# Kernel optimization log

Hardware: AMD Instinct MI355X
Metric: run time of the kernel (lower is better)

Reference implementation:

```python
import jax, jax.numpy as jnp
import numpy as np
from jax import lax

H = 300  # L1 = L2 = 300 in the source


def setup_inputs() -> dict:
    key = jax.random.key(0)
    ks = jax.random.split(key, 10)
    B = 1024
    oplen = 256
    s = 1.0 / np.sqrt(H)
    return {
        "h0": jax.random.normal(ks[0], (B, H), jnp.float32),
        "c0": jax.random.normal(ks[1], (B, H), jnp.float32),
        "start": jax.random.normal(ks[2], (B, H), jnp.float32),
        # LSTMCell params (PyTorch layout: [4H, H] weights, [4H] biases; gate order i,f,g,o)
        "W_ih": jax.random.normal(ks[3], (4 * H, H), jnp.float32) * s,
        "W_hh": jax.random.normal(ks[4], (4 * H, H), jnp.float32) * s,
        "b_ih": jax.random.normal(ks[5], (4 * H,), jnp.float32) * s,
        "b_hh": jax.random.normal(ks[6], (4 * H,), jnp.float32) * s,
        # output Linear [H, H]
        "W_out": jax.random.normal(ks[7], (H, H), jnp.float32) * s,
        "b_out": jax.random.normal(ks[8], (H,), jnp.float32) * s,
        "oplen": oplen,
    }


def reference(h0, c0, start, W_ih, W_hh, b_ih, b_hh, W_out, b_out, oplen):
    def step(carry, _):
        h, c, x = carry
        # LSTMCell: gates = x W_ih^T + b_ih + h W_hh^T + b_hh
        gates = x @ W_ih.T + b_ih + h @ W_hh.T + b_hh  # [B, 4H]
        i, f, g, o = jnp.split(gates, 4, axis=-1)
        i = jax.nn.sigmoid(i)
        f = jax.nn.sigmoid(f)
        g = jnp.tanh(g)
        o = jax.nn.sigmoid(o)
        c_new = f * c + i * g
        h_new = o * jnp.tanh(c_new)
        out = h_new @ W_out.T + b_out  # fed back as next input
        return (h_new, c_new, out), out

    _, outs = lax.scan(step, (h0, c0, start), None, length=oplen)
    return outs  # [oplen, B, H]
```

## Files before the change

### kernel.cpp

```cpp
#include <hip/hip_runtime.h>
#include <hip/hip_bf16.h>


typedef __attribute__((ext_vector_type(8))) short bf16x8;
typedef __attribute__((ext_vector_type(4))) float f32x4;

__device__ __forceinline__ float sigf(float x) { return 1.0f / (1.0f + __expf(-x)); }
__device__ __forceinline__ float tanh_fast(float x) { return 2.0f / (1.0f + __expf(-2.0f * x)) - 1.0f; }
__device__ __forceinline__ short f2bf(float x) { __hip_bfloat16 h = __float2bfloat16(x); return *(short*)&h; }
__device__ __forceinline__ float bf2f(short s) { __hip_bfloat16 h; *(short*)&h = s; return __bfloat162float(h); }

__global__ void build_kernel(const float* __restrict__ W_out, const float* __restrict__ b_out,
                             float* __restrict__ W_big, float* __restrict__ bias_big,
                             unsigned int* __restrict__ hfrag_zero) {
    int stride = gridDim.x * blockDim.x;
    int idx = blockIdx.x * blockDim.x + threadIdx.x;
    for (int i = idx; i < 655360; i += stride) hfrag_zero[i] = 0u;
    for (int i = idx; i < 300 * 300; i += stride) W_big[1200 * 300 + i] = W_out[i];
    for (int i = idx; i < 300; i += stride) bias_big[1200 + i] = b_out[i];
}

__global__ __launch_bounds__(128) void fold_kernel(const float* __restrict__ W_ih,
                                                   const float* __restrict__ W_hh,
                                                   const float* __restrict__ W_out,
                                                   float* __restrict__ W_big) {
    int j = blockIdx.x;
    __shared__ float row[300];
    for (int m = threadIdx.x; m < 300; m += 128) row[m] = W_ih[j * 300 + m];
    __syncthreads();
    int k0 = threadIdx.x, k1 = threadIdx.x + 128, k2 = threadIdx.x + 256;
    float a0 = 0.f, a1 = 0.f, a2 = 0.f;
    for (int m = 0; m < 300; ++m) {
        float w = row[m];
        a0 += w * W_out[m * 300 + k0];
        a1 += w * W_out[m * 300 + k1];
        if (k2 < 300) a2 += w * W_out[m * 300 + k2];
    }
    W_big[j * 300 + k0] = W_hh[j * 300 + k0] + a0;
    W_big[j * 300 + k1] = W_hh[j * 300 + k1] + a1;
    if (k2 < 300) W_big[j * 300 + k2] = W_hh[j * 300 + k2] + a2;
}

__global__ __launch_bounds__(64) void bias_fold_kernel(const float* __restrict__ W_ih,
                                                       const float* __restrict__ b_ih,
                                                       const float* __restrict__ b_hh,
                                                       const float* __restrict__ b_out,
                                                       float* __restrict__ bias_big) {
    int j = blockIdx.x;
    int lane = threadIdx.x;
    float s = 0.f;
    for (int m = lane; m < 300; m += 64) s += W_ih[j * 300 + m] * b_out[m];
    for (int off = 32; off > 0; off >>= 1) s += __shfl_down(s, off);
    if (lane == 0) bias_big[j] = b_ih[j] + b_hh[j] + s;
}

__global__ __launch_bounds__(64) void pack_w_kernel(const float* __restrict__ W_big,
                                                    short* __restrict__ Wh, short* __restrict__ Wl) {
    int tile = blockIdx.x;
    int jt = tile / 50;
    int rem = tile - jt * 50;
    int ch = rem / 10;
    int kc = rem - ch * 10;
    int lane = threadIdx.x;
    int j = jt * 16 + (lane & 15);
    int kbase = kc * 32 + (lane >> 4) * 8;
    int r = (ch < 4) ? (ch * 300 + j) : (1200 + j);
    size_t base = (size_t)tile * 512 + (size_t)lane * 8;
#pragma unroll
    for (int jj = 0; jj < 8; ++jj) {
        int k = kbase + jj;
        float v = (j < 300 && k < 300) ? W_big[(size_t)r * 300 + k] : 0.f;
        short hi = f2bf(v);
        short lo = f2bf(v - bf2f(hi));
        Wh[base + jj] = hi;
        Wl[base + jj] = lo;
    }
}

__global__ __launch_bounds__(128) void step0_kernel(
    const float* __restrict__ x_in, const float* __restrict__ h_in,
    const float* __restrict__ W_ih, const float* __restrict__ W_hh,
    const float* __restrict__ b_ih, const float* __restrict__ b_hh,
    const float* __restrict__ c_in, float* __restrict__ c_out,
    float* __restrict__ h_out) {
    __shared__ float hs[16][68];
    __shared__ float wsm[16][32];
    const int t = threadIdx.x;
    const int bm0 = blockIdx.x * 64;
    const int jg0 = blockIdx.y * 8;

    const int row_idx = t & 31;
    const int wkq = (t >> 5) << 2;
    const int jl = row_idx >> 2, g = row_idx & 3;
    const int grow = jg0 + jl + 300 * g;
    const bool wvalid = (jg0 + jl) < 300;

    float acc[4][4];
#pragma unroll
    for (int i = 0; i < 4; ++i)
#pragma unroll
        for (int q = 0; q < 4; ++q) acc[i][q] = 0.f;

    for (int it = 0; it < 38; ++it) {
        const int k0 = it << 4;
#pragma unroll
        for (int q = 0; q < 2; ++q) {
            int qi = t + q * 128;
            int bl = qi >> 2;
            int kq = (qi & 3) << 2;
            int kg = k0 + kq;
            float4 hv = make_float4(0.f, 0.f, 0.f, 0.f);
            if (kg < 600) {
                const float* src = (kg < 300) ? (x_in + (size_t)(bm0 + bl) * 300 + kg)
                                              : (h_in + (size_t)(bm0 + bl) * 300 + (kg - 300));
                hv = *(const float4*)src;
            }
            hs[kq + 0][bl] = hv.x;
            hs[kq + 1][bl] = hv.y;
            hs[kq + 2][bl] = hv.z;
            hs[kq + 3][bl] = hv.w;
        }
        {
            int kg = k0 + wkq;
            float4 wv = make_float4(0.f, 0.f, 0.f, 0.f);
            if (wvalid && kg < 600) {
                const float* src = (kg < 300) ? (W_ih + (size_t)grow * 300 + kg)
                                              : (W_hh + (size_t)grow * 300 + (kg - 300));
                wv = *(const float4*)src;
            }
            wsm[wkq + 0][row_idx] = wv.x;
            wsm[wkq + 1][row_idx] = wv.y;
            wsm[wkq + 2][row_idx] = wv.z;
            wsm[wkq + 3][row_idx] = wv.w;
        }
        __syncthreads();
        const int bs4 = (t & 15) << 2;
        const int c4 = (t >> 4) << 2;
#pragma unroll
        for (int k = 0; k < 16; ++k) {
            float4 hv = *(const float4*)&hs[k][bs4];
            float4 wv = *(const float4*)&wsm[k][c4];
            float hvv[4] = {hv.x, hv.y, hv.z, hv.w};
            float wvv[4] = {wv.x, wv.y, wv.z, wv.w};
#pragma unroll
            for (int bi = 0; bi < 4; ++bi)
#pragma unroll
                for (int q = 0; q < 4; ++q) acc[bi][q] += hvv[bi] * wvv[q];
        }
        __syncthreads();
    }

    const int b0 = bm0 + ((t & 15) << 2);
    const int j = jg0 + (t >> 4);
    if (j < 300) {
        const float bi_ = b_ih[j] + b_hh[j];
        const float bf_ = b_ih[j + 300] + b_hh[j + 300];
        const float bg_ = b_ih[j + 600] + b_hh[j + 600];
        const float bo_ = b_ih[j + 900] + b_hh[j + 900];
#pragma unroll
        for (int bi = 0; bi < 4; ++bi) {
            const int b = b0 + bi;
            float ig = sigf(acc[bi][0] + bi_);
            float fg = sigf(acc[bi][1] + bf_);
            float gg = tanh_fast(acc[bi][2] + bg_);
            float og = sigf(acc[bi][3] + bo_);
            float cn = fg * c_in[(size_t)b * 300 + j] + ig * gg;
            c_out[(size_t)b * 300 + j] = cn;
            h_out[(size_t)b * 300 + j] = og * tanh_fast(cn);
        }
    }
}

__global__ __launch_bounds__(256) void convert_h_kernel(const float* __restrict__ h_row,
                                                        short* __restrict__ Hh, short* __restrict__ Hl) {
    int idx = blockIdx.x * 256 + threadIdx.x;
    int m = idx / 320;
    int k = idx - m * 320;
    float v = (k < 300) ? h_row[(size_t)m * 300 + k] : 0.f;
    short hi = f2bf(v);
    short lo = f2bf(v - bf2f(hi));
    int chunk = k >> 5;
    int lane = (m & 15) + 16 * ((k & 31) >> 3);
    int slot = k & 7;
    size_t fi = (((size_t)(m >> 4) * 10 + chunk) * 64 + lane) * 8 + slot;
    Hh[fi] = hi;
    Hl[fi] = lo;
}

__global__ __launch_bounds__(192, 2) void step_kernel(
    const short* __restrict__ Ah, const short* __restrict__ Al,
    short* __restrict__ Bh, short* __restrict__ Bl,
    const short* __restrict__ Wh, const short* __restrict__ Wl,
    const float* __restrict__ bias,
    float* __restrict__ c_st,
    float* __restrict__ y_out) {
    const int bid = blockIdx.x;
    const int jt = bid >> 5;
    const int mxp = bid & 31;
    const int tid = threadIdx.x;
    const int wave = tid >> 6;
    const int lane = tid & 63;

    __shared__ short As_h[2 * 10 * 512];
    __shared__ short As_l[2 * 10 * 512];
    __shared__ float gbuf[4][32][16];

    {
        const size_t abase = (size_t)(mxp * 2) * 10 * 512;
        const int4* gAh = (const int4*)(Ah + abase);
        const int4* gAl = (const int4*)(Al + abase);
        int4* sAh = (int4*)As_h;
        int4* sAl = (int4*)As_l;
        for (int i = tid; i < 1280; i += 192) {
            sAh[i] = gAh[i];
            sAl[i] = gAl[i];
        }
    }
    __syncthreads();

    const short* aoff_h = As_h + lane * 8;
    const short* aoff_l = As_l + lane * 8;

    if (wave < 2) {
        const int ch0 = wave * 2;
        f32x4 acc[2][2];
#pragma unroll
        for (int a = 0; a < 2; ++a)
#pragma unroll
            for (int b = 0; b < 2; ++b) acc[a][b] = (f32x4){0.f, 0.f, 0.f, 0.f};

        const short* wb_h[2] = {Wh + ((size_t)(jt * 5 + ch0) * 10) * 512 + lane * 8,
                                Wh + ((size_t)(jt * 5 + ch0 + 1) * 10) * 512 + lane * 8};
        const short* wb_l[2] = {Wl + ((size_t)(jt * 5 + ch0) * 10) * 512 + lane * 8,
                                Wl + ((size_t)(jt * 5 + ch0 + 1) * 10) * 512 + lane * 8};
#pragma unroll 2
        for (int kc = 0; kc < 10; ++kc) {
            bf16x8 a0h = *(const bf16x8*)(aoff_h + kc * 512);
            bf16x8 a0l = *(const bf16x8*)(aoff_l + kc * 512);
            bf16x8 a1h = *(const bf16x8*)(aoff_h + (10 + kc) * 512);
            bf16x8 a1l = *(const bf16x8*)(aoff_l + (10 + kc) * 512);
#pragma unroll
            for (int chl = 0; chl < 2; ++chl) {
                bf16x8 bh = *(const bf16x8*)(wb_h[chl] + kc * 512);
                bf16x8 bl = *(const bf16x8*)(wb_l[chl] + kc * 512);
                acc[chl][0] = __builtin_amdgcn_mfma_f32_16x16x32_bf16(a0h, bh, acc[chl][0], 0, 0, 0);
                acc[chl][0] = __builtin_amdgcn_mfma_f32_16x16x32_bf16(a0l, bh, acc[chl][0], 0, 0, 0);
                acc[chl][0] = __builtin_amdgcn_mfma_f32_16x16x32_bf16(a0h, bl, acc[chl][0], 0, 0, 0);
                acc[chl][1] = __builtin_amdgcn_mfma_f32_16x16x32_bf16(a1h, bh, acc[chl][1], 0, 0, 0);
                acc[chl][1] = __builtin_amdgcn_mfma_f32_16x16x32_bf16(a1l, bh, acc[chl][1], 0, 0, 0);
                acc[chl][1] = __builtin_amdgcn_mfma_f32_16x16x32_bf16(a1h, bl, acc[chl][1], 0, 0, 0);
            }
        }
        const int jl = lane & 15;
        const int mr = (lane >> 4) * 4;
#pragma unroll
        for (int chl = 0; chl < 2; ++chl)
#pragma unroll
            for (int mt = 0; mt < 2; ++mt)
#pragma unroll
                for (int r = 0; r < 4; ++r)
                    gbuf[ch0 + chl][mt * 16 + mr + r][jl] = acc[chl][mt][r];
    } else {
        f32x4 accy[2];
        accy[0] = (f32x4){0.f, 0.f, 0.f, 0.f};
        accy[1] = (f32x4){0.f, 0.f, 0.f, 0.f};
        const short* wy = Wh + ((size_t)(jt * 5 + 4) * 10) * 512 + lane * 8;
#pragma unroll 2
        for (int kc = 0; kc < 10; ++kc) {
            bf16x8 a0h = *(const bf16x8*)(aoff_h + kc * 512);
            bf16x8 a0l = *(const bf16x8*)(aoff_l + kc * 512);
            bf16x8 a1h = *(const bf16x8*)(aoff_h + (10 + kc) * 512);
            bf16x8 a1l = *(const bf16x8*)(aoff_l + (10 + kc) * 512);
            bf16x8 bh = *(const bf16x8*)(wy + kc * 512);
            accy[0] = __builtin_amdgcn_mfma_f32_16x16x32_bf16(a0h, bh, accy[0], 0, 0, 0);
            accy[0] = __builtin_amdgcn_mfma_f32_16x16x32_bf16(a0l, bh, accy[0], 0, 0, 0);
            accy[1] = __builtin_amdgcn_mfma_f32_16x16x32_bf16(a1h, bh, accy[1], 0, 0, 0);
            accy[1] = __builtin_amdgcn_mfma_f32_16x16x32_bf16(a1l, bh, accy[1], 0, 0, 0);
        }
        const int j = jt * 16 + (lane & 15);
        if (j < 300) {
            const float by = bias[1200 + j];
            const int mr = (lane >> 4) * 4;
#pragma unroll
            for (int mt = 0; mt < 2; ++mt)
#pragma unroll
                for (int r = 0; r < 4; ++r) {
                    const int m = mxp * 32 + mt * 16 + mr + r;
                    y_out[(size_t)m * 300 + j] = accy[mt][r] + by;
                }
        }
    }
    __syncthreads();

    for (int e = tid; e < 512; e += 192) {
        const int ml = e >> 4;
        const int jl = e & 15;
        const int j = jt * 16 + jl;
        if (j >= 300) continue;
        const int m = mxp * 32 + ml;
        float gi = gbuf[0][ml][jl] + bias[j];
        float gf = gbuf[1][ml][jl] + bias[300 + j];
        float gg = gbuf[2][ml][jl] + bias[600 + j];
        float go = gbuf[3][ml][jl] + bias[900 + j];
        float iv = sigf(gi), fv = sigf(gf), gv = tanh_fast(gg), ov = sigf(go);
        const size_t cj = (size_t)m * 300 + j;
        float cn = fv * c_st[cj] + iv * gv;
        c_st[cj] = cn;
        float hv = ov * tanh_fast(cn);
        short hb = f2bf(hv);
        short lb = f2bf(hv - bf2f(hb));
        const int chunk = j >> 5;
        const int lane_a = (m & 15) + 16 * ((j & 31) >> 3);
        const int slot = j & 7;
        const size_t fi = (((size_t)(m >> 4) * 10 + chunk) * 64 + lane_a) * 8 + slot;
        Bh[fi] = hb;
        Bl[fi] = lb;
    }
}

extern "C" void kernel_launch(void* const* d_in, const int* in_sizes, int n_in,
                              void* d_out, int out_size, void* d_ws, size_t ws_size,
                              hipStream_t stream) {
    const float* h0 = (const float*)d_in[0];
    const float* c0 = (const float*)d_in[1];
    const float* start = (const float*)d_in[2];
    const float* W_ih = (const float*)d_in[3];
    const float* W_hh = (const float*)d_in[4];
    const float* b_ih = (const float*)d_in[5];
    const float* b_hh = (const float*)d_in[6];
    const float* W_out = (const float*)d_in[7];
    const float* b_out = (const float*)d_in[8];
    float* out = (float*)d_out;

    float* wsf = (float*)d_ws;
    float* W_big = wsf;
    float* bias_big = wsf + 450000;
    float* c_ws = wsf + 451504;
    float* h_row = wsf + 758704;
    short* wss = (short*)(wsf + 1065904);
    short* Wh = wss;
    short* Wl = wss + 486400;
    short* H0h = wss + 972800;
    short* H0l = wss + 1300480;
    short* H1h = wss + 1628160;
    short* H1l = wss + 1955840;

    build_kernel<<<2816, 256, 0, stream>>>(W_out, b_out, W_big, bias_big, (unsigned int*)H0h);
    fold_kernel<<<1200, 128, 0, stream>>>(W_ih, W_hh, W_out, W_big);
    bias_fold_kernel<<<1200, 64, 0, stream>>>(W_ih, b_ih, b_hh, b_out, bias_big);
    pack_w_kernel<<<950, 64, 0, stream>>>(W_big, Wh, Wl);

    step0_kernel<<<dim3(16, 38), 128, 0, stream>>>(start, h0, W_ih, W_hh, b_ih, b_hh,
                                                   c0, c_ws, h_row);
    convert_h_kernel<<<1280, 256, 0, stream>>>(h_row, H0h, H0l);

    short* Hb[2][2] = {{H0h, H0l}, {H1h, H1l}};
    for (int tt = 1; tt <= 256; ++tt) {
        short** A = Hb[(tt - 1) & 1];
        short** Bn = Hb[tt & 1];
        step_kernel<<<608, 192, 0, stream>>>(A[0], A[1], Bn[0], Bn[1], Wh, Wl,
                                             bias_big, c_ws,
                                             out + (size_t)(tt - 1) * 307200);
    }
}
```

Before: 2.424 ms.

## Replace per-step launches with persistent kernel using grid barrier and LDS-resident weights

Replaces the 256 per-timestep step_kernel launches with one persistent kernel of 247 blocks that loops over all timesteps, separated by a global atomic barrier. Each block keeps its weight slice (hi/lo bf16) in LDS, keeps its cell state in registers, and double-buffers loading of the h fragments from global memory into LDS. The tiling changes to 80 rows by 16 columns per block. This removes launch overhead and repeated weight/c-state traffic, at the cost of a spin barrier whose correctness depends on all 247 blocks being co-resident.

```diff
diff --git a/kernel.cpp b/kernel.cpp
--- a/kernel.cpp
+++ b/kernel.cpp
@@ -4,6 +4,8 @@
 
 typedef __attribute__((ext_vector_type(8))) short bf16x8;
 typedef __attribute__((ext_vector_type(4))) float f32x4;
+
+#define MFMA16(a, b, c) __builtin_amdgcn_mfma_f32_16x16x32_bf16((a), (b), (c), 0, 0, 0)
 
 __device__ __forceinline__ float sigf(float x) { return 1.0f / (1.0f + __expf(-x)); }
 __device__ __forceinline__ float tanh_fast(float x) { return 2.0f / (1.0f + __expf(-2.0f * x)) - 1.0f; }
@@ -12,12 +14,13 @@
 
 __global__ void build_kernel(const float* __restrict__ W_out, const float* __restrict__ b_out,
                              float* __restrict__ W_big, float* __restrict__ bias_big,
-                             unsigned int* __restrict__ hfrag_zero) {
+                             unsigned int* __restrict__ hfrag_zero, unsigned int* __restrict__ bar) {
     int stride = gridDim.x * blockDim.x;
     int idx = blockIdx.x * blockDim.x + threadIdx.x;
-    for (int i = idx; i < 655360; i += stride) hfrag_zero[i] = 0u;
+    for (int i = idx; i < 665600; i += stride) hfrag_zero[i] = 0u;
     for (int i = idx; i < 300 * 300; i += stride) W_big[1200 * 300 + i] = W_out[i];
     for (int i = idx; i < 300; i += stride) bias_big[1200 + i] = b_out[i];
+    if (idx < 64) bar[idx] = 0u;
 }
 
 __global__ __launch_bounds__(128) void fold_kernel(const float* __restrict__ W_ih,
@@ -187,134 +190,227 @@
     Hl[fi] = lo;
 }
 
-__global__ __launch_bounds__(192, 2) void step_kernel(
-    const short* __restrict__ Ah, const short* __restrict__ Al,
-    short* __restrict__ Bh, short* __restrict__ Bl,
-    const short* __restrict__ Wh, const short* __restrict__ Wl,
-    const float* __restrict__ bias,
-    float* __restrict__ c_st,
-    float* __restrict__ y_out) {
+__global__ __launch_bounds__(256, 1) void persist_kernel(
+    short* __restrict__ H0h, short* __restrict__ H0l,
+    short* __restrict__ H1h, short* __restrict__ H1l,
+    const short* __restrict__ Wph, const short* __restrict__ Wpl,
+    const float* __restrict__ bias, const float* __restrict__ c_init,
+    float* __restrict__ out, unsigned int* __restrict__ bar) {
+    __shared__ __align__(16) short w_hi[5 * 10 * 512];
+    __shared__ __align__(16) short w_lo[4 * 10 * 512];
+    __shared__ __align__(16) short a_sm[2 * 2 * 2 * 5 * 512];
+    __shared__ float gbuf[5][80][17];
+    __shared__ float bias_s[80];
+
     const int bid = blockIdx.x;
-    const int jt = bid >> 5;
-    const int mxp = bid & 31;
+    const int seq = (bid & 7) * 31 + (bid >> 3);
+    const int mg = seq / 19;
+    const int jt = seq - mg * 19;
     const int tid = threadIdx.x;
     const int wave = tid >> 6;
     const int lane = tid & 63;
 
-    __shared__ short As_h[2 * 10 * 512];
-    __shared__ short As_l[2 * 10 * 512];
-    __shared__ float gbuf[4][32][16];
-
     {
-        const size_t abase = (size_t)(mxp * 2) * 10 * 512;
-        const int4* gAh = (const int4*)(Ah + abase);
-        const int4* gAl = (const int4*)(Al + abase);
-        int4* sAh = (int4*)As_h;
-        int4* sAl = (int4*)As_l;
-        for (int i = tid; i < 1280; i += 192) {
-            sAh[i] = gAh[i];
-            sAl[i] = gAl[i];
-        }
-    }
-    __syncthreads();
-
-    const short* aoff_h = As_h + lane * 8;
-    const short* aoff_l = As_l + lane * 8;
-
-    if (wave < 2) {
-        const int ch0 = wave * 2;
-        f32x4 acc[2][2];
-#pragma unroll
-        for (int a = 0; a < 2; ++a)
-#pragma unroll
-            for (int b = 0; b < 2; ++b) acc[a][b] = (f32x4){0.f, 0.f, 0.f, 0.f};
-
-        const short* wb_h[2] = {Wh + ((size_t)(jt * 5 + ch0) * 10) * 512 + lane * 8,
-                                Wh + ((size_t)(jt * 5 + ch0 + 1) * 10) * 512 + lane * 8};
-        const short* wb_l[2] = {Wl + ((size_t)(jt * 5 + ch0) * 10) * 512 + lane * 8,
-                                Wl + ((size_t)(jt * 5 + ch0 + 1) * 10) * 512 + lane * 8};
-#pragma unroll 2
-        for (int kc = 0; kc < 10; ++kc) {
-            bf16x8 a0h = *(const bf16x8*)(aoff_h + kc * 512);
-            bf16x8 a0l = *(const bf16x8*)(aoff_l + kc * 512);
-            bf16x8 a1h = *(const bf16x8*)(aoff_h + (10 + kc) * 512);
-            bf16x8 a1l = *(const bf16x8*)(aoff_l + (10 + kc) * 512);
-#pragma unroll
-            for (int chl = 0; chl < 2; ++chl) {
-                bf16x8 bh = *(const bf16x8*)(wb_h[chl] + kc * 512);
-                bf16x8 bl = *(const bf16x8*)(wb_l[chl] + kc * 512);
-                acc[chl][0] = __builtin_amdgcn_mfma_f32_16x16x32_bf16(a0h, bh, acc[chl][0], 0, 0, 0);
-                acc[chl][0] = __builtin_amdgcn_mfma_f32_16x16x32_bf16(a0l, bh, acc[chl][0], 0, 0, 0);
-                acc[chl][0] = __builtin_amdgcn_mfma_f32_16x16x32_bf16(a0h, bl, acc[chl][0], 0, 0, 0);
-                acc[chl][1] = __builtin_amdgcn_mfma_f32_16x16x32_bf16(a1h, bh, acc[chl][1], 0, 0, 0);
-                acc[chl][1] = __builtin_amdgcn_mfma_f32_16x16x32_bf16(a1l, bh, acc[chl][1], 0, 0, 0);
-                acc[chl][1] = __builtin_amdgcn_mfma_f32_16x16x32_bf16(a1h, bl, acc[chl][1], 0, 0, 0);
-            }
-        }
-        const int jl = lane & 15;
-        const int mr = (lane >> 4) * 4;
-#pragma unroll
-        for (int chl = 0; chl < 2; ++chl)
-#pragma unroll
-            for (int mt = 0; mt < 2; ++mt)
-#pragma unroll
-                for (int r = 0; r < 4; ++r)
-                    gbuf[ch0 + chl][mt * 16 + mr + r][jl] = acc[chl][mt][r];
-    } else {
-        f32x4 accy[2];
-        accy[0] = (f32x4){0.f, 0.f, 0.f, 0.f};
-        accy[1] = (f32x4){0.f, 0.f, 0.f, 0.f};
-        const short* wy = Wh + ((size_t)(jt * 5 + 4) * 10) * 512 + lane * 8;
-#pragma unroll 2
-        for (int kc = 0; kc < 10; ++kc) {
-            bf16x8 a0h = *(const bf16x8*)(aoff_h + kc * 512);
-            bf16x8 a0l = *(const bf16x8*)(aoff_l + kc * 512);
-            bf16x8 a1h = *(const bf16x8*)(aoff_h + (10 + kc) * 512);
-            bf16x8 a1l = *(const bf16x8*)(aoff_l + (10 + kc) * 512);
-            bf16x8 bh = *(const bf16x8*)(wy + kc * 512);
-            accy[0] = __builtin_amdgcn_mfma_f32_16x16x32_bf16(a0h, bh, accy[0], 0, 0, 0);
-            accy[0] = __builtin_amdgcn_mfma_f32_16x16x32_bf16(a0l, bh, accy[0], 0, 0, 0);
-            accy[1] = __builtin_amdgcn_mfma_f32_16x16x32_bf16(a1h, bh, accy[1], 0, 0, 0);
-            accy[1] = __builtin_amdgcn_mfma_f32_16x16x32_bf16(a1l, bh, accy[1], 0, 0, 0);
-        }
-        const int j = jt * 16 + (lane & 15);
-        if (j < 300) {
-            const float by = bias[1200 + j];
-            const int mr = (lane >> 4) * 4;
-#pragma unroll
-            for (int mt = 0; mt < 2; ++mt)
-#pragma unroll
-                for (int r = 0; r < 4; ++r) {
-                    const int m = mxp * 32 + mt * 16 + mr + r;
-                    y_out[(size_t)m * 300 + j] = accy[mt][r] + by;
-                }
-        }
-    }
-    __syncthreads();
-
-    for (int e = tid; e < 512; e += 192) {
-        const int ml = e >> 4;
-        const int jl = e & 15;
+        const int4* s1 = (const int4*)(Wph + (size_t)jt * 25600);
+        int4* d1 = (int4*)w_hi;
+        for (int i = tid; i < 3200; i += 256) d1[i] = s1[i];
+        const int4* s2 = (const int4*)(Wpl + (size_t)jt * 25600);
+        int4* d2 = (int4*)w_lo;
+        for (int i = tid; i < 2560; i += 256) d2[i] = s2[i];
+        if (tid < 80) {
+            const int cch = tid >> 4, jl = tid & 15;
+            const int j = jt * 16 + jl;
+            bias_s[tid] = (j < 300) ? bias[cch * 300 + j] : 0.f;
+        }
+    }
+
+    float c_reg[5];
+#pragma unroll
+    for (int k = 0; k < 5; ++k) {
+        const int e = tid + (k << 8);
+        const int ml = e >> 4, jl = e & 15;
         const int j = jt * 16 + jl;
-        if (j >= 300) continue;
-        const int m = mxp * 32 + ml;
-        float gi = gbuf[0][ml][jl] + bias[j];
-        float gf = gbuf[1][ml][jl] + bias[300 + j];
-        float gg = gbuf[2][ml][jl] + bias[600 + j];
-        float go = gbuf[3][ml][jl] + bias[900 + j];
-        float iv = sigf(gi), fv = sigf(gf), gv = tanh_fast(gg), ov = sigf(go);
-        const size_t cj = (size_t)m * 300 + j;
-        float cn = fv * c_st[cj] + iv * gv;
-        c_st[cj] = cn;
-        float hv = ov * tanh_fast(cn);
-        short hb = f2bf(hv);
-        short lb = f2bf(hv - bf2f(hb));
-        const int chunk = j >> 5;
-        const int lane_a = (m & 15) + 16 * ((j & 31) >> 3);
-        const int slot = j & 7;
-        const size_t fi = (((size_t)(m >> 4) * 10 + chunk) * 64 + lane_a) * 8 + slot;
-        Bh[fi] = hb;
-        Bl[fi] = lb;
+        const int m = mg * 80 + ml;
+        c_reg[k] = (j < 300 && m < 1024) ? c_init[(size_t)m * 300 + j] : 0.f;
+    }
+
+    const int chb = (wave >> 1) << 1;
+    const int gmlo = (wave & 1) ? 3 : 0;
+    const int gcnt = (wave & 1) ? 2 : 3;
+    const int ycnt = (wave == 1) ? 2 : ((wave == 3) ? 3 : 0);
+    const int ymlo = (wave == 1) ? 3 : 0;
+
+    const short* whB = w_hi + chb * 5120 + (lane << 3);
+    const short* wlB = w_lo + chb * 5120 + (lane << 3);
+    const short* wyB = w_hi + 4 * 5120 + (lane << 3);
+    const short* aB = a_sm + (lane << 3);
+
+    const int jlc = lane & 15;
+    const int mr = ((lane >> 4) << 2);
+
+#pragma unroll 1
+    for (int tt = 1; tt <= 256; ++tt) {
+        const short* Ah = (tt & 1) ? H0h : H1h;
+        const short* Al = (tt & 1) ? H0l : H1l;
+        short* Bh = (tt & 1) ? H1h : H0h;
+        short* Bl = (tt & 1) ? H1l : H0l;
+        float* yo = out + (size_t)(tt - 1) * 307200;
+
+        f32x4 acc[2][3];
+        f32x4 accy[3];
+#pragma unroll
+        for (int c = 0; c < 2; ++c)
+#pragma unroll
+            for (int i = 0; i < 3; ++i) acc[c][i] = (f32x4){0.f, 0.f, 0.f, 0.f};
+#pragma unroll
+        for (int i = 0; i < 3; ++i) accy[i] = (f32x4){0.f, 0.f, 0.f, 0.f};
+
+        {
+            int4 st[5];
+#pragma unroll
+            for (int i = 0; i < 5; ++i) {
+                const int o = wave + (i << 2);
+                const int mt = o % 5, prec = (o / 5) & 1, kcL = o / 10;
+                const short* src = prec ? Al : Ah;
+                st[i] = ((const int4*)(src + ((size_t)((mg * 5 + mt) * 10 + kcL) << 9)))[lane];
+            }
+#pragma unroll
+            for (int i = 0; i < 5; ++i) {
+                const int o = wave + (i << 2);
+                const int mt = o % 5, prec = (o / 5) & 1, kcL = o / 10;
+                ((int4*)(a_sm + ((size_t)((((kcL << 1) | prec) * 5 + mt)) << 9)))[lane] = st[i];
+            }
+        }
+        __syncthreads();
+
+#pragma unroll
+        for (int nc = 0; nc < 5; ++nc) {
+            const int rb = nc & 1;
+            int4 st[5];
+            if (nc < 4) {
+#pragma unroll
+                for (int i = 0; i < 5; ++i) {
+                    const int o = wave + (i << 2);
+                    const int mt = o % 5, prec = (o / 5) & 1, kcL = o / 10;
+                    const short* src = prec ? Al : Ah;
+                    st[i] = ((const int4*)(src +
+                              ((size_t)((mg * 5 + mt) * 10 + (nc * 2 + 2 + kcL)) << 9)))[lane];
+                }
+            }
+#pragma unroll
+            for (int kcL = 0; kcL < 2; ++kcL) {
+                const int kc = nc * 2 + kcL;
+                const bf16x8 bh0 = *(const bf16x8*)(whB + (kc << 9));
+                const bf16x8 bh1 = *(const bf16x8*)(whB + ((10 + kc) << 9));
+                const bf16x8 bl0 = *(const bf16x8*)(wlB + (kc << 9));
+                const bf16x8 bl1 = *(const bf16x8*)(wlB + ((10 + kc) << 9));
+                const short* ab = aB + (((rb << 1) | kcL) * 5120);
+#pragma unroll
+                for (int mti = 0; mti < 3; ++mti) {
+                    if (mti < gcnt) {
+                        const int mt = gmlo + mti;
+                        const bf16x8 ah = *(const bf16x8*)(ab + (mt << 9));
+                        const bf16x8 al = *(const bf16x8*)(ab + ((5 + mt) << 9));
+                        acc[0][mti] = MFMA16(ah, bh0, acc[0][mti]);
+                        acc[0][mti] = MFMA16(al, bh0, acc[0][mti]);
+                        acc[0][mti] = MFMA16(ah, bl0, acc[0][mti]);
+                        acc[1][mti] = MFMA16(ah, bh1, acc[1][mti]);
+                        acc[1][mti] = MFMA16(al, bh1, acc[1][mti]);
+                        acc[1][mti] = MFMA16(ah, bl1, acc[1][mti]);
+                    }
+                }
+                if (ycnt) {
+                    const bf16x8 byh = *(const bf16x8*)(wyB + (kc << 9));
+#pragma unroll
+                    for (int yi = 0; yi < 3; ++yi) {
+                        if (yi < ycnt) {
+                            const int mt = ymlo + yi;
+                            const bf16x8 ah = *(const bf16x8*)(ab + (mt << 9));
+                            const bf16x8 al = *(const bf16x8*)(ab + ((5 + mt) << 9));
+                            accy[yi] = MFMA16(ah, byh, accy[yi]);
+                            accy[yi] = MFMA16(al, byh, accy[yi]);
+                        }
+                    }
+                }
+            }
+            if (nc < 4) {
+                const int wb = rb ^ 1;
+#pragma unroll
+                for (int i = 0; i < 5; ++i) {
+                    const int o = wave + (i << 2);
+                    const int mt = o % 5, prec = (o / 5) & 1, kcL = o / 10;
+                    ((int4*)(a_sm + ((size_t)(((((wb << 1) | kcL) << 1) | prec) * 5 + mt) << 9)))[lane] = st[i];
+                }
+            }
+            __syncthreads();
+        }
+
+#pragma unroll
+        for (int c = 0; c < 2; ++c)
+#pragma unroll
+            for (int mti = 0; mti < 3; ++mti) {
+                if (mti < gcnt) {
+#pragma unroll
+                    for (int r = 0; r < 4; ++r)
+                        gbuf[chb + c][(gmlo + mti) * 16 + mr + r][jlc] = acc[c][mti][r];
+                }
+            }
+        if (ycnt) {
+#pragma unroll
+            for (int yi = 0; yi < 3; ++yi) {
+                if (yi < ycnt) {
+#pragma unroll
+                    for (int r = 0; r < 4; ++r)
+                        gbuf[4][(ymlo + yi) * 16 + mr + r][jlc] = accy[yi][r];
+                }
+            }
+        }
+        __syncthreads();
+
+#pragma unroll
+        for (int k = 0; k < 5; ++k) {
+            const int e = tid + (k << 8);
+            const int ml = e >> 4, jl = e & 15;
+            const int j = jt * 16 + jl;
+            const int m = mg * 80 + ml;
+            if (j < 300 && m < 1024) {
+                const float gi = gbuf[0][ml][jl] + bias_s[jl];
+                const float gf = gbuf[1][ml][jl] + bias_s[16 + jl];
+                const float gg = gbuf[2][ml][jl] + bias_s[32 + jl];
+                const float go_ = gbuf[3][ml][jl] + bias_s[48 + jl];
+                const float iv = sigf(gi), fv = sigf(gf), gv = tanh_fast(gg), ov = sigf(go_);
+                const float cn = fv * c_reg[k] + iv * gv;
+                c_reg[k] = cn;
+                const float hv = ov * tanh_fast(cn);
+                const float yv = gbuf[4][ml][jl] + bias_s[64 + jl];
+                __builtin_nontemporal_store(yv, yo + (size_t)m * 300 + j);
+                const short hb = f2bf(hv);
+                const short lb = f2bf(hv - bf2f(hb));
+                const int chk = j >> 5;
+                const int lane_a = (m & 15) + (((j & 31) >> 3) << 4);
+                const int slot = j & 7;
+                const size_t fi = ((((size_t)(m >> 4) * 10 + chk) << 6) + lane_a) * 8 + slot;
+                __builtin_nontemporal_store(hb, Bh + fi);
+                __builtin_nontemporal_store(lb, Bl + fi);
+            }
+        }
+
+        __syncthreads();
+        if (tid == 0) {
+            __threadfence();
+            const unsigned prev =
+                __hip_atomic_fetch_add(&bar[0], 1u, __ATOMIC_RELAXED, __HIP_MEMORY_SCOPE_AGENT);
+            if (prev == (unsigned)(247 * tt - 1)) {
+                __hip_atomic_store(&bar[32], (unsigned)tt, __ATOMIC_RELAXED, __HIP_MEMORY_SCOPE_AGENT);
+            } else {
+                while (__hip_atomic_load(&bar[32], __ATOMIC_RELAXED, __HIP_MEMORY_SCOPE_AGENT) <
+                       (unsigned)tt) {
+                    __builtin_amdgcn_s_sleep(2);
+                }
+            }
+            __threadfence();
+        }
+        __syncthreads();
     }
 }
 
@@ -341,11 +437,12 @@
     short* Wh = wss;
     short* Wl = wss + 486400;
     short* H0h = wss + 972800;
-    short* H0l = wss + 1300480;
-    short* H1h = wss + 1628160;
-    short* H1l = wss + 1955840;
-
-    build_kernel<<<2816, 256, 0, stream>>>(W_out, b_out, W_big, bias_big, (unsigned int*)H0h);
+    short* H0l = wss + 1305600;
+    short* H1h = wss + 1638400;
+    short* H1l = wss + 1971200;
+    unsigned int* bar = (unsigned int*)(wss + 2304000);
+
+    build_kernel<<<2816, 256, 0, stream>>>(W_out, b_out, W_big, bias_big, (unsigned int*)H0h, bar);
     fold_kernel<<<1200, 128, 0, stream>>>(W_ih, W_hh, W_out, W_big);
     bias_fold_kernel<<<1200, 64, 0, stream>>>(W_ih, b_ih, b_hh, b_out, bias_big);
     pack_w_kernel<<<950, 64, 0, stream>>>(W_big, Wh, Wl);
@@ -354,12 +451,6 @@
                                                    c0, c_ws, h_row);
     convert_h_kernel<<<1280, 256, 0, stream>>>(h_row, H0h, H0l);
 
-    short* Hb[2][2] = {{H0h, H0l}, {H1h, H1l}};
-    for (int tt = 1; tt <= 256; ++tt) {
-        short** A = Hb[(tt - 1) & 1];
-        short** Bn = Hb[tt & 1];
-        step_kernel<<<608, 192, 0, stream>>>(A[0], A[1], Bn[0], Bn[1], Wh, Wl,
-                                             bias_big, c_ws,
-                                             out + (size_t)(tt - 1) * 307200);
-    }
-}
+    persist_kernel<<<247, 256, 0, stream>>>(H0h, H0l, H1h, H1l, Wh, Wl,
+                                            bias_big, c_ws, out, bar);
+}
```

Measured after the change: 5.927 ms. +144.5%, slower.

## Replace per-step launches with persistent kernel using per-group flag synchronization

Applied to the files above, without the earlier changes.

Swaps 256 separate step launches for one persistent kernel of 152 blocks. Blocks are split into 8 groups of 19, each owning 128 batch rows, and the blocks of a group coordinate through atomic step flags in global memory. Each block keeps its slice of the packed weights in LDS and the cell state in registers. The aim is to remove per-step launch overhead and the repeated weight and state reloads, at the cost of spin-wait polling and reliance on all blocks being co-resident.

```diff
diff --git a/kernel.cpp b/kernel.cpp
--- a/kernel.cpp
+++ b/kernel.cpp
@@ -4,6 +4,8 @@
 
 typedef __attribute__((ext_vector_type(8))) short bf16x8;
 typedef __attribute__((ext_vector_type(4))) float f32x4;
+
+#define MFMA16(a, b, c) __builtin_amdgcn_mfma_f32_16x16x32_bf16((a), (b), (c), 0, 0, 0)
 
 __device__ __forceinline__ float sigf(float x) { return 1.0f / (1.0f + __expf(-x)); }
 __device__ __forceinline__ float tanh_fast(float x) { return 2.0f / (1.0f + __expf(-2.0f * x)) - 1.0f; }
@@ -12,12 +14,13 @@
 
 __global__ void build_kernel(const float* __restrict__ W_out, const float* __restrict__ b_out,
                              float* __restrict__ W_big, float* __restrict__ bias_big,
-                             unsigned int* __restrict__ hfrag_zero) {
+                             unsigned int* __restrict__ hfrag_zero, unsigned int* __restrict__ flags) {
     int stride = gridDim.x * blockDim.x;
     int idx = blockIdx.x * blockDim.x + threadIdx.x;
     for (int i = idx; i < 655360; i += stride) hfrag_zero[i] = 0u;
     for (int i = idx; i < 300 * 300; i += stride) W_big[1200 * 300 + i] = W_out[i];
     for (int i = idx; i < 300; i += stride) bias_big[1200 + i] = b_out[i];
+    if (idx < 256) flags[idx] = 0u;
 }
 
 __global__ __launch_bounds__(128) void fold_kernel(const float* __restrict__ W_ih,
@@ -187,134 +190,174 @@
     Hl[fi] = lo;
 }
 
-__global__ __launch_bounds__(192, 2) void step_kernel(
-    const short* __restrict__ Ah, const short* __restrict__ Al,
-    short* __restrict__ Bh, short* __restrict__ Bl,
-    const short* __restrict__ Wh, const short* __restrict__ Wl,
-    const float* __restrict__ bias,
-    float* __restrict__ c_st,
-    float* __restrict__ y_out) {
+__global__ __launch_bounds__(256, 1) void persist_kernel(
+    short* __restrict__ H0h, short* __restrict__ H0l,
+    short* __restrict__ H1h, short* __restrict__ H1l,
+    const short* __restrict__ Wph, const short* __restrict__ Wpl,
+    const float* __restrict__ bias, const float* __restrict__ c_init,
+    float* __restrict__ out, unsigned* __restrict__ flags) {
+    __shared__ __align__(16) short w_hi[50 * 512];
+    __shared__ __align__(16) short w_lo[40 * 512];
+
     const int bid = blockIdx.x;
-    const int jt = bid >> 5;
-    const int mxp = bid & 31;
+    const int g = bid / 19;
+    const int jt = bid - g * 19;
     const int tid = threadIdx.x;
     const int wave = tid >> 6;
     const int lane = tid & 63;
 
-    __shared__ short As_h[2 * 10 * 512];
-    __shared__ short As_l[2 * 10 * 512];
-    __shared__ float gbuf[4][32][16];
-
     {
-        const size_t abase = (size_t)(mxp * 2) * 10 * 512;
-        const int4* gAh = (const int4*)(Ah + abase);
-        const int4* gAl = (const int4*)(Al + abase);
-        int4* sAh = (int4*)As_h;
-        int4* sAl = (int4*)As_l;
-        for (int i = tid; i < 1280; i += 192) {
-            sAh[i] = gAh[i];
-            sAl[i] = gAl[i];
-        }
-    }
+        const int4* s1 = (const int4*)(Wph + (size_t)jt * 25600);
+        int4* d1 = (int4*)w_hi;
+        for (int i = tid; i < 3200; i += 256) d1[i] = s1[i];
+        const int4* s2 = (const int4*)(Wpl + (size_t)jt * 25600);
+        int4* d2 = (int4*)w_lo;
+        for (int i = tid; i < 2560; i += 256) d2[i] = s2[i];
+    }
+
+    const int jl = lane & 15;
+    const int jg = jt * 16 + jl;
+    const bool jvalid = jg < 300;
+    const int mr = (lane >> 4) << 2;
+    const int laneo = lane << 3;
+
+    float b_i = 0.f, b_f = 0.f, b_g = 0.f, b_o = 0.f, b_y = 0.f;
+    if (jvalid) {
+        b_i = bias[jg];
+        b_f = bias[300 + jg];
+        b_g = bias[600 + jg];
+        b_o = bias[900 + jg];
+        b_y = bias[1200 + jg];
+    }
+
+    const int mt0 = g * 8 + wave;
+    float c_reg[8];
+#pragma unroll
+    for (int mti = 0; mti < 2; ++mti)
+#pragma unroll
+        for (int r = 0; r < 4; ++r) {
+            const int m = (mt0 + 4 * mti) * 16 + mr + r;
+            c_reg[mti * 4 + r] = jvalid ? c_init[(size_t)m * 300 + jg] : 0.f;
+        }
+
+    const int iA = mt0 * 640 + lane;
+    const int chunk = jt >> 1;
+    const int halfA = 2 * (jt & 1) + (jl >> 3);
+    const int sloti = jl & 7;
+    unsigned* fpoll_p = flags + (g * 19 + (lane < 19 ? lane : 18));
+    unsigned* fpub_p = flags + (g * 19 + jt);
+
     __syncthreads();
 
-    const short* aoff_h = As_h + lane * 8;
-    const short* aoff_l = As_l + lane * 8;
-
-    if (wave < 2) {
-        const int ch0 = wave * 2;
-        f32x4 acc[2][2];
-#pragma unroll
-        for (int a = 0; a < 2; ++a)
-#pragma unroll
-            for (int b = 0; b < 2; ++b) acc[a][b] = (f32x4){0.f, 0.f, 0.f, 0.f};
-
-        const short* wb_h[2] = {Wh + ((size_t)(jt * 5 + ch0) * 10) * 512 + lane * 8,
-                                Wh + ((size_t)(jt * 5 + ch0 + 1) * 10) * 512 + lane * 8};
-        const short* wb_l[2] = {Wl + ((size_t)(jt * 5 + ch0) * 10) * 512 + lane * 8,
-                                Wl + ((size_t)(jt * 5 + ch0 + 1) * 10) * 512 + lane * 8};
-#pragma unroll 2
-        for (int kc = 0; kc < 10; ++kc) {
-            bf16x8 a0h = *(const bf16x8*)(aoff_h + kc * 512);
-            bf16x8 a0l = *(const bf16x8*)(aoff_l + kc * 512);
-            bf16x8 a1h = *(const bf16x8*)(aoff_h + (10 + kc) * 512);
-            bf16x8 a1l = *(const bf16x8*)(aoff_l + (10 + kc) * 512);
-#pragma unroll
-            for (int chl = 0; chl < 2; ++chl) {
-                bf16x8 bh = *(const bf16x8*)(wb_h[chl] + kc * 512);
-                bf16x8 bl = *(const bf16x8*)(wb_l[chl] + kc * 512);
-                acc[chl][0] = __builtin_amdgcn_mfma_f32_16x16x32_bf16(a0h, bh, acc[chl][0], 0, 0, 0);
-                acc[chl][0] = __builtin_amdgcn_mfma_f32_16x16x32_bf16(a0l, bh, acc[chl][0], 0, 0, 0);
-                acc[chl][0] = __builtin_amdgcn_mfma_f32_16x16x32_bf16(a0h, bl, acc[chl][0], 0, 0, 0);
-                acc[chl][1] = __builtin_amdgcn_mfma_f32_16x16x32_bf16(a1h, bh, acc[chl][1], 0, 0, 0);
-                acc[chl][1] = __builtin_amdgcn_mfma_f32_16x16x32_bf16(a1l, bh, acc[chl][1], 0, 0, 0);
-                acc[chl][1] = __builtin_amdgcn_mfma_f32_16x16x32_bf16(a1h, bl, acc[chl][1], 0, 0, 0);
-            }
-        }
-        const int jl = lane & 15;
-        const int mr = (lane >> 4) * 4;
-#pragma unroll
-        for (int chl = 0; chl < 2; ++chl)
-#pragma unroll
-            for (int mt = 0; mt < 2; ++mt)
-#pragma unroll
-                for (int r = 0; r < 4; ++r)
-                    gbuf[ch0 + chl][mt * 16 + mr + r][jl] = acc[chl][mt][r];
-    } else {
+#pragma unroll 1
+    for (int tt = 1; tt <= 256; ++tt) {
+        const short* Ah8 = (tt & 1) ? H0h : H1h;
+        const short* Al8 = (tt & 1) ? H0l : H1l;
+        short* Bh8 = (tt & 1) ? H1h : H0h;
+        short* Bl8 = (tt & 1) ? H1l : H0l;
+        float* yo = out + (size_t)(tt - 1) * 307200;
+
+        if (tt > 1) {
+            if (wave == 0) {
+                const unsigned target = (unsigned)(tt - 1);
+                while (true) {
+                    unsigned fv = __hip_atomic_load(fpoll_p, __ATOMIC_RELAXED,
+                                                    __HIP_MEMORY_SCOPE_AGENT);
+                    if (__all((int)((lane >= 19) | (fv >= target)))) break;
+                    __builtin_amdgcn_s_sleep(1);
+                }
+                __threadfence();
+            }
+            __syncthreads();
+        }
+
+        const int4* A4h = (const int4*)Ah8 + iA;
+        const int4* A4l = (const int4*)Al8 + iA;
+
+        f32x4 acc[4][2];
         f32x4 accy[2];
+#pragma unroll
+        for (int ch = 0; ch < 4; ++ch) {
+            acc[ch][0] = (f32x4){0.f, 0.f, 0.f, 0.f};
+            acc[ch][1] = (f32x4){0.f, 0.f, 0.f, 0.f};
+        }
         accy[0] = (f32x4){0.f, 0.f, 0.f, 0.f};
         accy[1] = (f32x4){0.f, 0.f, 0.f, 0.f};
-        const short* wy = Wh + ((size_t)(jt * 5 + 4) * 10) * 512 + lane * 8;
-#pragma unroll 2
+
+        int4 p0h[3], p0l[3], p1h[3], p1l[3];
+        p0h[0] = A4h[0];
+        p0l[0] = A4l[0];
+        p1h[0] = A4h[2560];
+        p1l[0] = A4l[2560];
+        p0h[1] = A4h[64];
+        p0l[1] = A4l[64];
+        p1h[1] = A4h[2624];
+        p1l[1] = A4l[2624];
+
+#pragma unroll
         for (int kc = 0; kc < 10; ++kc) {
-            bf16x8 a0h = *(const bf16x8*)(aoff_h + kc * 512);
-            bf16x8 a0l = *(const bf16x8*)(aoff_l + kc * 512);
-            bf16x8 a1h = *(const bf16x8*)(aoff_h + (10 + kc) * 512);
-            bf16x8 a1l = *(const bf16x8*)(aoff_l + (10 + kc) * 512);
-            bf16x8 bh = *(const bf16x8*)(wy + kc * 512);
-            accy[0] = __builtin_amdgcn_mfma_f32_16x16x32_bf16(a0h, bh, accy[0], 0, 0, 0);
-            accy[0] = __builtin_amdgcn_mfma_f32_16x16x32_bf16(a0l, bh, accy[0], 0, 0, 0);
-            accy[1] = __builtin_amdgcn_mfma_f32_16x16x32_bf16(a1h, bh, accy[1], 0, 0, 0);
-            accy[1] = __builtin_amdgcn_mfma_f32_16x16x32_bf16(a1l, bh, accy[1], 0, 0, 0);
-        }
-        const int j = jt * 16 + (lane & 15);
-        if (j < 300) {
-            const float by = bias[1200 + j];
-            const int mr = (lane >> 4) * 4;
-#pragma unroll
-            for (int mt = 0; mt < 2; ++mt)
-#pragma unroll
-                for (int r = 0; r < 4; ++r) {
-                    const int m = mxp * 32 + mt * 16 + mr + r;
-                    y_out[(size_t)m * 300 + j] = accy[mt][r] + by;
+            const int cs = kc % 3;
+            if (kc + 2 < 10) {
+                const int ns = (kc + 2) % 3;
+                p0h[ns] = A4h[(kc + 2) * 64];
+                p0l[ns] = A4l[(kc + 2) * 64];
+                p1h[ns] = A4h[2560 + (kc + 2) * 64];
+                p1l[ns] = A4l[2560 + (kc + 2) * 64];
+            }
+            const bf16x8 a0h = *(const bf16x8*)&p0h[cs];
+            const bf16x8 a0l = *(const bf16x8*)&p0l[cs];
+            const bf16x8 a1h = *(const bf16x8*)&p1h[cs];
+            const bf16x8 a1l = *(const bf16x8*)&p1l[cs];
+#pragma unroll
+            for (int ch = 0; ch < 4; ++ch) {
+                const bf16x8 bh = *(const bf16x8*)(w_hi + ((ch * 10 + kc) << 9) + laneo);
+                const bf16x8 bl = *(const bf16x8*)(w_lo + ((ch * 10 + kc) << 9) + laneo);
+                acc[ch][0] = MFMA16(a0h, bh, acc[ch][0]);
+                acc[ch][0] = MFMA16(a0l, bh, acc[ch][0]);
+                acc[ch][0] = MFMA16(a0h, bl, acc[ch][0]);
+                acc[ch][1] = MFMA16(a1h, bh, acc[ch][1]);
+                acc[ch][1] = MFMA16(a1l, bh, acc[ch][1]);
+                acc[ch][1] = MFMA16(a1h, bl, acc[ch][1]);
+            }
+            const bf16x8 by = *(const bf16x8*)(w_hi + ((40 + kc) << 9) + laneo);
+            accy[0] = MFMA16(a0h, by, accy[0]);
+            accy[0] = MFMA16(a0l, by, accy[0]);
+            accy[1] = MFMA16(a1h, by, accy[1]);
+            accy[1] = MFMA16(a1l, by, accy[1]);
+        }
+
+#pragma unroll
+        for (int mti = 0; mti < 2; ++mti) {
+            const int MT = mt0 + 4 * mti;
+#pragma unroll
+            for (int r = 0; r < 4; ++r) {
+                const float gi = acc[0][mti][r] + b_i;
+                const float gf = acc[1][mti][r] + b_f;
+                const float gg = acc[2][mti][r] + b_g;
+                const float go_ = acc[3][mti][r] + b_o;
+                const float iv = sigf(gi), fv = sigf(gf), gv = tanh_fast(gg), ov = sigf(go_);
+                const float cn = fv * c_reg[mti * 4 + r] + iv * gv;
+                c_reg[mti * 4 + r] = cn;
+                const float hv = ov * tanh_fast(cn);
+                if (jvalid) {
+                    const int m = MT * 16 + mr + r;
+                    __builtin_nontemporal_store(accy[mti][r] + b_y, yo + (size_t)m * 300 + jg);
+                    const short hb = f2bf(hv);
+                    const short lb = f2bf(hv - bf2f(hb));
+                    const int lane_a = (mr + r) + (halfA << 4);
+                    const size_t fi = (((size_t)(MT * 10 + chunk) << 6) + lane_a) * 8 + sloti;
+                    Bh8[fi] = hb;
+                    Bl8[fi] = lb;
                 }
-        }
-    }
-    __syncthreads();
-
-    for (int e = tid; e < 512; e += 192) {
-        const int ml = e >> 4;
-        const int jl = e & 15;
-        const int j = jt * 16 + jl;
-        if (j >= 300) continue;
-        const int m = mxp * 32 + ml;
-        float gi = gbuf[0][ml][jl] + bias[j];
-        float gf = gbuf[1][ml][jl] + bias[300 + j];
-        float gg = gbuf[2][ml][jl] + bias[600 + j];
-        float go = gbuf[3][ml][jl] + bias[900 + j];
-        float iv = sigf(gi), fv = sigf(gf), gv = tanh_fast(gg), ov = sigf(go);
-        const size_t cj = (size_t)m * 300 + j;
-        float cn = fv * c_st[cj] + iv * gv;
-        c_st[cj] = cn;
-        float hv = ov * tanh_fast(cn);
-        short hb = f2bf(hv);
-        short lb = f2bf(hv - bf2f(hb));
-        const int chunk = j >> 5;
-        const int lane_a = (m & 15) + 16 * ((j & 31) >> 3);
-        const int slot = j & 7;
-        const size_t fi = (((size_t)(m >> 4) * 10 + chunk) * 64 + lane_a) * 8 + slot;
-        Bh[fi] = hb;
-        Bl[fi] = lb;
+            }
+        }
+
+        __syncthreads();
+        if (tid == 0) {
+            __threadfence();
+            __hip_atomic_store(fpub_p, (unsigned)tt, __ATOMIC_RELAXED,
+                               __HIP_MEMORY_SCOPE_AGENT);
+        }
     }
 }
 
@@ -344,8 +387,9 @@
     short* H0l = wss + 1300480;
     short* H1h = wss + 1628160;
     short* H1l = wss + 1955840;
-
-    build_kernel<<<2816, 256, 0, stream>>>(W_out, b_out, W_big, bias_big, (unsigned int*)H0h);
+    unsigned* flags = (unsigned*)(wss + 2283520);
+
+    build_kernel<<<2816, 256, 0, stream>>>(W_out, b_out, W_big, bias_big, (unsigned int*)H0h, flags);
     fold_kernel<<<1200, 128, 0, stream>>>(W_ih, W_hh, W_out, W_big);
     bias_fold_kernel<<<1200, 64, 0, stream>>>(W_ih, b_ih, b_hh, b_out, bias_big);
     pack_w_kernel<<<950, 64, 0, stream>>>(W_big, Wh, Wl);
@@ -354,12 +398,6 @@
                                                    c0, c_ws, h_row);
     convert_h_kernel<<<1280, 256, 0, stream>>>(h_row, H0h, H0l);
 
-    short* Hb[2][2] = {{H0h, H0l}, {H1h, H1l}};
-    for (int tt = 1; tt <= 256; ++tt) {
-        short** A = Hb[(tt - 1) & 1];
-        short** Bn = Hb[tt & 1];
-        step_kernel<<<608, 192, 0, stream>>>(A[0], A[1], Bn[0], Bn[1], Wh, Wl,
-                                             bias_big, c_ws,
-                                             out + (size_t)(tt - 1) * 307200);
-    }
-}
+    persist_kernel<<<152, 256, 0, stream>>>(H0h, H0l, H1h, H1l, Wh, Wl,
+                                            bias_big, c_ws, out, flags);
+}
```

Measured after the change: 5.133 ms. +111.8%, slower.
